# Performance work log

Measured on AMD Instinct MI355X. Metric: run time of the kernel, lower is better.

The kernel has to match this reference:

```python
import math
import jax, jax.numpy as jnp
import numpy as np

B, S, H, BOT, RD, N, K = 4, 2048, 1024, 128, 48, 4096, 8

def setup_inputs() -> dict:
    key = jax.random.key(0)
    ks = jax.random.split(key, 12)
    hidden_states = jax.random.normal(ks[0], (B, S, H), jnp.float32)
    q_proj_w = jax.random.normal(ks[1], (BOT, H), jnp.float32) * (1.0 / math.sqrt(H))
    router_w = jax.random.normal(ks[2], (RD, BOT), jnp.float32) * (1.0 / math.sqrt(BOT))
    aux_keys = jax.random.normal(ks[3], (N, BOT), jnp.float32) * 0.01
    aux_values = jax.random.normal(ks[4], (N, H), jnp.float32) * 0.02
    # reliability per slot (log-domain additive mask derived from lifecycle state)
    reliability_mask = jax.random.uniform(ks[5], (N,), jnp.float32)
    unc_w1 = jax.random.normal(ks[6], (H // 4, H), jnp.float32) * (1.0 / math.sqrt(H))
    unc_b1 = jnp.zeros((H // 4,), jnp.float32)
    unc_w2 = jax.random.normal(ks[7], (1, H // 4), jnp.float32) * 0.02
    unc_b2 = jnp.zeros((1,), jnp.float32)
    gate_w1 = jnp.asarray(0.5, jnp.float32)
    gate_bias = jnp.asarray(-1.0, jnp.float32)
    return {"hidden_states": hidden_states, "q_proj_w": q_proj_w, "router_w": router_w,
            "aux_keys": aux_keys, "aux_values": aux_values, "reliability_mask": reliability_mask,
            "unc_w1": unc_w1, "unc_b1": unc_b1, "unc_w2": unc_w2, "unc_b2": unc_b2,
            "gate_w1": gate_w1, "gate_bias": gate_bias}

def reference(hidden_states, q_proj_w, router_w, aux_keys, aux_values, reliability_mask,
              unc_w1, unc_b1, unc_w2, unc_b2, gate_w1, gate_bias):
    # --- SlotRouter: project query/keys to router_dim, score, mask, top-k ---
    query = jnp.einsum('bsh,dh->bsd', hidden_states, q_proj_w)        # [B,S,BOT]
    rq = jnp.einsum('bsd,rd->bsr', query, router_w)                   # [B,S,RD]
    rk = jnp.einsum('nd,rd->nr', aux_keys, router_w)                  # [N,RD]
    scores = jnp.einsum('bsr,nr->bsn', rq, rk) / math.sqrt(RD)        # [B,S,N]
    scores = scores + reliability_mask[None, None, :]
    top_scores, top_idx = jax.lax.top_k(scores, K)                    # [B,S,K]
    # --- UncertaintyEstimator (HIDDEN_VARIANCE) ---
    mean = hidden_states.mean(axis=-1, keepdims=True)
    variance = ((hidden_states - mean) ** 2).mean(axis=-1)            # [B,S]
    log_var = jnp.log1p(variance)
    normalized_var = log_var / (log_var.mean() + 1e-6)
    h1 = jax.nn.gelu(jnp.einsum('bsh,fh->bsf', hidden_states, unc_w1) + unc_b1, approximate=False)
    learned = (jnp.einsum('bsf,of->bso', h1, unc_w2) + unc_b2)[..., 0]
    uncertainty = jnp.clip(normalized_var * 0.5 + jax.nn.sigmoid(learned) * 2.5, 0.0, 5.0)
    # --- Gate-1 scalar gate + slot aggregation ---
    gate = jax.nn.sigmoid(gate_w1 * uncertainty + gate_bias)          # [B,S]
    w = jax.nn.softmax(top_scores, axis=-1)                           # [B,S,K]
    v = aux_values[top_idx]                                           # [B,S,K,H]
    agg = jnp.einsum('bsk,bskh->bsh', w, v)
    out = hidden_states + gate[..., None] * agg
    return out
```

## Files before the change

kernel.cpp:

```cpp
#include <hip/hip_runtime.h>
#include <hip/hip_bf16.h>
#include <math.h>
#include <stdint.h>

#define NT 256
constexpr int Hc = 1024, BOTc = 128, RDc = 48, Nc = 4096;
constexpr int ROWS = 8192;
constexpr float INV_SQRT_RD = 0.14433756729740643f;

typedef short bf16x8 __attribute__((ext_vector_type(8)));
typedef float f32x4 __attribute__((ext_vector_type(4)));

__device__ __forceinline__ uint32_t umin32(uint32_t a, uint32_t b) { return a < b ? a : b; }
__device__ __forceinline__ uint32_t umax32(uint32_t a, uint32_t b) { return a > b ? a : b; }
__device__ __forceinline__ void ce_asc(uint32_t& x, uint32_t& y) {
  uint32_t lo = umin32(x, y), hi = umax32(x, y); x = lo; y = hi;
}
__device__ __forceinline__ uint32_t pack_score(float s, int slot) {
  uint32_t u = __float_as_uint(s);
  u = (u & 0x80000000u) ? ~u : (u | 0x80000000u);
  return (u & 0xFFFFF000u) | (uint32_t)slot;
}
__device__ __forceinline__ float unpack_score(uint32_t p) {
  uint32_t m = p & 0xFFFFF000u;
  uint32_t f = (m & 0x80000000u) ? (m ^ 0x80000000u) : ~m;
  return __uint_as_float(f);
}
__device__ __forceinline__ void merge_top8(uint32_t a[8], const uint32_t b[8]) {
  uint32_t m[8];
#pragma unroll
  for (int i = 0; i < 8; ++i) m[i] = umax32(a[i], b[7 - i]);
  ce_asc(m[0], m[4]); ce_asc(m[1], m[5]); ce_asc(m[2], m[6]); ce_asc(m[3], m[7]);
  ce_asc(m[0], m[2]); ce_asc(m[1], m[3]); ce_asc(m[4], m[6]); ce_asc(m[5], m[7]);
  ce_asc(m[0], m[1]); ce_asc(m[2], m[3]); ce_asc(m[4], m[5]); ce_asc(m[6], m[7]);
#pragma unroll
  for (int i = 0; i < 8; ++i) a[i] = m[i];
}
__device__ __forceinline__ void top8_insert(uint32_t top[8], uint32_t p) {
  if (p > top[0]) {
    top[0] = p;
    ce_asc(top[0], top[1]); ce_asc(top[1], top[2]); ce_asc(top[2], top[3]);
    ce_asc(top[3], top[4]); ce_asc(top[4], top[5]); ce_asc(top[5], top[6]);
    ce_asc(top[6], top[7]);
  }
}
__device__ __forceinline__ uint16_t bf16bits(float x) {
  uint32_t u = __float_as_uint(x);
  return (uint16_t)(((u + 0x7FFFu + ((u >> 16) & 1u)) >> 16) & 0xFFFFu);
}
__device__ __forceinline__ float bf2f(uint16_t h) {
  return __uint_as_float((uint32_t)h << 16);
}

constexpr int GP_W48 = 64, GP_RK = 768, GP_HB = 1024, GP_CVW = 32, GP_CVA = 512;
__global__ __launch_bounds__(256) void k_prep_all(
    const float* __restrict__ hidden, const float* __restrict__ q_proj_w,
    const float* __restrict__ router_w, const float* __restrict__ aux_keys,
    const float* __restrict__ aux_values, const float* __restrict__ rel,
    const float* __restrict__ unc_w1,
    uint16_t* __restrict__ xb, float* __restrict__ log_var,
    uint16_t* __restrict__ wcat, uint16_t* __restrict__ avb,
    uint16_t* __restrict__ rk_b) {
  int bid = blockIdx.x;
  int tid = threadIdx.x;
  if (bid < GP_W48) {
    __shared__ float rw[BOTc];
    int j = bid;
    if (j >= RDc) {
      for (int hh = tid; hh < Hc; hh += NT) wcat[(size_t)(256 + j) * Hc + hh] = 0;
      return;
    }
    for (int d = tid; d < BOTc; d += NT) rw[d] = router_w[j * BOTc + d];
    __syncthreads();
    float acc[4] = {0.f, 0.f, 0.f, 0.f};
#pragma unroll 4
    for (int d = 0; d < BOTc; ++d) {
      float r = rw[d];
#pragma unroll
      for (int jj = 0; jj < 4; ++jj)
        acc[jj] = fmaf(r, q_proj_w[d * Hc + tid + 256 * jj], acc[jj]);
    }
#pragma unroll
    for (int jj = 0; jj < 4; ++jj)
      wcat[(size_t)(256 + j) * Hc + tid + 256 * jj] = bf16bits(acc[jj]);
    return;
  }
  bid -= GP_W48;
  if (bid < GP_RK) {
    int gid = bid * NT + tid;
    int n = gid / RDc, r = gid - n * RDc;
    float acc = 0.f;
#pragma unroll 8
    for (int d = 0; d < BOTc; ++d)
      acc = fmaf(aux_keys[n * BOTc + d], router_w[r * BOTc + d], acc);
    rk_b[(size_t)n * 64 + r] = bf16bits(acc * INV_SQRT_RD);
    if (r < 16) rk_b[(size_t)n * 64 + 48 + r] = (r == 0) ? bf16bits(rel[n]) : (uint16_t)0;
    return;
  }
  bid -= GP_RK;
  if (bid < GP_HB) {
    int wave = tid >> 6, lane = tid & 63;
    int row = bid * 8 + wave * 2;
    const float4* r0 = reinterpret_cast<const float4*>(hidden + (size_t)row * Hc);
    const float4* r1 = reinterpret_cast<const float4*>(hidden + (size_t)(row + 1) * Hc);
    float4 v0[4], v1[4];
#pragma unroll
    for (int i = 0; i < 4; ++i) v0[i] = r0[lane + 64 * i];
#pragma unroll
    for (int i = 0; i < 4; ++i) v1[i] = r1[lane + 64 * i];
    float s0 = 0.f, q0 = 0.f, s1 = 0.f, q1 = 0.f;
#pragma unroll
    for (int i = 0; i < 4; ++i) {
      ushort4 h;
      h.x = bf16bits(v0[i].x); h.y = bf16bits(v0[i].y);
      h.z = bf16bits(v0[i].z); h.w = bf16bits(v0[i].w);
      *reinterpret_cast<ushort4*>(xb + (size_t)row * Hc + (lane + 64 * i) * 4) = h;
      s0 += v0[i].x + v0[i].y + v0[i].z + v0[i].w;
      q0 += v0[i].x * v0[i].x + v0[i].y * v0[i].y + v0[i].z * v0[i].z + v0[i].w * v0[i].w;
    }
#pragma unroll
    for (int i = 0; i < 4; ++i) {
      ushort4 h;
      h.x = bf16bits(v1[i].x); h.y = bf16bits(v1[i].y);
      h.z = bf16bits(v1[i].z); h.w = bf16bits(v1[i].w);
      *reinterpret_cast<ushort4*>(xb + (size_t)(row + 1) * Hc + (lane + 64 * i) * 4) = h;
      s1 += v1[i].x + v1[i].y + v1[i].z + v1[i].w;
      q1 += v1[i].x * v1[i].x + v1[i].y * v1[i].y + v1[i].z * v1[i].z + v1[i].w * v1[i].w;
    }
#pragma unroll
    for (int d = 32; d >= 1; d >>= 1) {
      s0 += __shfl_down(s0, d); q0 += __shfl_down(q0, d);
      s1 += __shfl_down(s1, d); q1 += __shfl_down(q1, d);
    }
    if (lane == 0) {
      float m0 = s0 * (1.f / Hc), m1 = s1 * (1.f / Hc);
      log_var[row]     = log1pf(q0 * (1.f / Hc) - m0 * m0);
      log_var[row + 1] = log1pf(q1 * (1.f / Hc) - m1 * m1);
    }
    return;
  }
  bid -= GP_HB;
  if (bid < GP_CVW) {
    float4 v[8];
    int base = bid * 2048 + tid;
#pragma unroll
    for (int i = 0; i < 8; ++i) v[i] = reinterpret_cast<const float4*>(unc_w1)[base + i * 256];
#pragma unroll
    for (int i = 0; i < 8; ++i) {
      ushort4 h;
      h.x = bf16bits(v[i].x); h.y = bf16bits(v[i].y);
      h.z = bf16bits(v[i].z); h.w = bf16bits(v[i].w);
      reinterpret_cast<ushort4*>(wcat)[base + i * 256] = h;
    }
    return;
  }
  bid -= GP_CVW;
  {
    float4 v[8];
    int base = bid * 2048 + tid;
#pragma unroll
    for (int i = 0; i < 8; ++i) v[i] = reinterpret_cast<const float4*>(aux_values)[base + i * 256];
#pragma unroll
    for (int i = 0; i < 8; ++i) {
      ushort4 h;
      h.x = bf16bits(v[i].x); h.y = bf16bits(v[i].y);
      h.z = bf16bits(v[i].z); h.w = bf16bits(v[i].w);
      reinterpret_cast<ushort4*>(avb)[base + i * 256] = h;
    }
  }
}

__global__ __launch_bounds__(256) void k_xw(const uint16_t* __restrict__ xb,
                                            const uint16_t* __restrict__ wcat,
                                            const float* __restrict__ b1,
                                            const float* __restrict__ w2,
                                            float* __restrict__ uncp,
                                            uint16_t* __restrict__ rq_b) {
  __shared__ uint16_t As[2][64 * 72];
  __shared__ uint16_t Bs[2][64 * 72];
  int bid = blockIdx.x;
  int wid = (bid & 7) * 80 + (bid >> 3);
  int rowg = wid / 5, colg = wid - rowg * 5;
  int tid = threadIdx.x, wave = tid >> 6, lane = tid & 63;
  int l15 = lane & 15, lg = lane >> 4;
  int wr = wave >> 1, wc = wave & 1;
  int row0 = rowg * 64, n0 = colg * 64;
  int srow = tid >> 3, sseg = tid & 7;
  const uint16_t* agp = xb + (size_t)(row0 + srow) * Hc + sseg * 8;
  const uint16_t* bgp = wcat + (size_t)(n0 + srow) * Hc + sseg * 8;
  int sboff = srow * 72 + sseg * 8;
  int arow = wr * 32 + l15, brow = wc * 32 + l15;

  bf16x8 ra0 = *reinterpret_cast<const bf16x8*>(agp);
  bf16x8 ra1 = *reinterpret_cast<const bf16x8*>(agp + (size_t)32 * Hc);
  bf16x8 rb0 = *reinterpret_cast<const bf16x8*>(bgp);
  bf16x8 rb1 = *reinterpret_cast<const bf16x8*>(bgp + (size_t)32 * Hc);
  f32x4 acc00 = {0.f,0.f,0.f,0.f}, acc01 = {0.f,0.f,0.f,0.f};
  f32x4 acc10 = {0.f,0.f,0.f,0.f}, acc11 = {0.f,0.f,0.f,0.f};

  for (int t = 0; t < 16; ++t) {
    int buf = t & 1;
    *reinterpret_cast<bf16x8*>(&As[buf][sboff]) = ra0;
    *reinterpret_cast<bf16x8*>(&As[buf][sboff + 32 * 72]) = ra1;
    *reinterpret_cast<bf16x8*>(&Bs[buf][sboff]) = rb0;
    *reinterpret_cast<bf16x8*>(&Bs[buf][sboff + 32 * 72]) = rb1;
    if (t < 15) {
      int k0 = (t + 1) * 64;
      ra0 = *reinterpret_cast<const bf16x8*>(agp + k0);
      ra1 = *reinterpret_cast<const bf16x8*>(agp + (size_t)32 * Hc + k0);
      rb0 = *reinterpret_cast<const bf16x8*>(bgp + k0);
      rb1 = *reinterpret_cast<const bf16x8*>(bgp + (size_t)32 * Hc + k0);
    }
    __syncthreads();
#pragma unroll
    for (int ks = 0; ks < 2; ++ks) {
      bf16x8 a0 = *reinterpret_cast<const bf16x8*>(&As[buf][arow * 72 + ks * 32 + lg * 8]);
      bf16x8 a1 = *reinterpret_cast<const bf16x8*>(&As[buf][(arow + 16) * 72 + ks * 32 + lg * 8]);
      bf16x8 b0 = *reinterpret_cast<const bf16x8*>(&Bs[buf][brow * 72 + ks * 32 + lg * 8]);
      bf16x8 b1f = *reinterpret_cast<const bf16x8*>(&Bs[buf][(brow + 16) * 72 + ks * 32 + lg * 8]);
      acc00 = __builtin_amdgcn_mfma_f32_16x16x32_bf16(a0, b0, acc00, 0, 0, 0);
      acc01 = __builtin_amdgcn_mfma_f32_16x16x32_bf16(a0, b1f, acc01, 0, 0, 0);
      acc10 = __builtin_amdgcn_mfma_f32_16x16x32_bf16(a1, b0, acc10, 0, 0, 0);
      acc11 = __builtin_amdgcn_mfma_f32_16x16x32_bf16(a1, b1f, acc11, 0, 0, 0);
    }
    __syncthreads();
  }
  if (colg < 4) {
    int gc0 = n0 + wc * 32 + l15;
    float b1v0 = b1[gc0],      w2v0 = w2[gc0];
    float b1v1 = b1[gc0 + 16], w2v1 = w2[gc0 + 16];
    int strip = colg * 2 + wc;
    float part0[4], part1[4];
#pragma unroll
    for (int r = 0; r < 4; ++r) {
      float x00 = acc00[r] + b1v0, x01 = acc01[r] + b1v1;
      float x10 = acc10[r] + b1v0, x11 = acc11[r] + b1v1;
      float g00 = 0.5f * x00 * (1.f + erff(x00 * 0.70710678118654752f));
      float g01 = 0.5f * x01 * (1.f + erff(x01 * 0.70710678118654752f));
      float g10 = 0.5f * x10 * (1.f + erff(x10 * 0.70710678118654752f));
      float g11 = 0.5f * x11 * (1.f + erff(x11 * 0.70710678118654752f));
      part0[r] = fmaf(g00, w2v0, g01 * w2v1);
      part1[r] = fmaf(g10, w2v0, g11 * w2v1);
    }
#pragma unroll
    for (int d = 1; d < 16; d <<= 1)
#pragma unroll
      for (int r = 0; r < 4; ++r) {
        part0[r] += __shfl_xor(part0[r], d);
        part1[r] += __shfl_xor(part1[r], d);
      }
    if (l15 == 0) {
#pragma unroll
      for (int r = 0; r < 4; ++r) {
        uncp[(size_t)(row0 + wr * 32 + lg * 4 + r) * 8 + strip] = part0[r];
        uncp[(size_t)(row0 + wr * 32 + 16 + lg * 4 + r) * 8 + strip] = part1[r];
      }
    }
  } else {
    int colA = wc * 32 + l15, colB = colA + 16;
#pragma unroll
    for (int r = 0; r < 4; ++r) {
      int rA = row0 + wr * 32 + lg * 4 + r, rB = rA + 16;
      uint16_t vA = bf16bits(acc00[r]);
      uint16_t vB = (colB == 48) ? (uint16_t)0x3F80u : bf16bits(acc01[r]);
      uint16_t uA = bf16bits(acc10[r]);
      uint16_t uB = (colB == 48) ? (uint16_t)0x3F80u : bf16bits(acc11[r]);
      rq_b[(size_t)rA * 64 + colA] = vA;
      rq_b[(size_t)rA * 64 + colB] = vB;
      rq_b[(size_t)rB * 64 + colA] = uA;
      rq_b[(size_t)rB * 64 + colB] = uB;
    }
  }
}

__global__ __launch_bounds__(256) void k_scores_mfma(const uint16_t* __restrict__ rq_b,
                                                     const uint16_t* __restrict__ rk_b,
                                                     uint32_t* __restrict__ cand,
                                                     const float* __restrict__ log_var,
                                                     float* __restrict__ stats) {
  int tid = threadIdx.x;
  if (blockIdx.x == 1024) {
    float s = 0.f;
    for (int i = tid; i < ROWS; i += NT) s += log_var[i];
#pragma unroll
    for (int d = 32; d >= 1; d >>= 1) s += __shfl_down(s, d);
    __shared__ float ls[4];
    int lane = tid & 63, wid = tid >> 6;
    if (lane == 0) ls[wid] = s;
    __syncthreads();
    if (tid == 0) {
      s = ls[0] + ls[1] + ls[2] + ls[3];
      stats[0] = 1.f / (s * (1.f / ROWS) + 1e-6f);
    }
    return;
  }
  int wave = tid >> 6, lane = tid & 63;
  int l15 = lane & 15, lg = lane >> 4;
  int rowg = blockIdx.x >> 3, range = blockIdx.x & 7;
  int q0 = rowg * 64 + wave * 16;
  const uint16_t* qp = rq_b + (size_t)(q0 + l15) * 64 + lg * 8;
  bf16x8 qf1 = *reinterpret_cast<const bf16x8*>(qp);
  bf16x8 qf2 = *reinterpret_cast<const bf16x8*>(qp + 32);
  uint32_t top[8];
#pragma unroll
  for (int q = 0; q < 8; ++q) top[q] = 0u;
  int sbase = range * 512;
  const uint16_t* kp = rk_b + (size_t)(sbase + l15) * 64 + lg * 8;
  bf16x8 a1c = *reinterpret_cast<const bf16x8*>(kp);
  bf16x8 a2c = *reinterpret_cast<const bf16x8*>(kp + 32);
  bf16x8 a3c = *reinterpret_cast<const bf16x8*>(kp + 1024);
  bf16x8 a4c = *reinterpret_cast<const bf16x8*>(kp + 1024 + 32);
#pragma unroll
  for (int t = 0; t < 32; t += 2) {
    bf16x8 a1n, a2n, a3n, a4n;
    if (t < 30) {
      const uint16_t* kpn = kp + (size_t)(t + 2) * 1024;
      a1n = *reinterpret_cast<const bf16x8*>(kpn);
      a2n = *reinterpret_cast<const bf16x8*>(kpn + 32);
      a3n = *reinterpret_cast<const bf16x8*>(kpn + 1024);
      a4n = *reinterpret_cast<const bf16x8*>(kpn + 1024 + 32);
    }
    int s0 = sbase + t * 16;
    f32x4 acc0 = {0.f,0.f,0.f,0.f}, acc1 = {0.f,0.f,0.f,0.f};
    acc0 = __builtin_amdgcn_mfma_f32_16x16x32_bf16(a1c, qf1, acc0, 0, 0, 0);
    acc1 = __builtin_amdgcn_mfma_f32_16x16x32_bf16(a3c, qf1, acc1, 0, 0, 0);
    acc0 = __builtin_amdgcn_mfma_f32_16x16x32_bf16(a2c, qf2, acc0, 0, 0, 0);
    acc1 = __builtin_amdgcn_mfma_f32_16x16x32_bf16(a4c, qf2, acc1, 0, 0, 0);
#pragma unroll
    for (int r = 0; r < 4; ++r) top8_insert(top, pack_score(acc0[r], s0 + lg * 4 + r));
#pragma unroll
    for (int r = 0; r < 4; ++r) top8_insert(top, pack_score(acc1[r], s0 + 16 + lg * 4 + r));
    if (t < 30) { a1c = a1n; a2c = a2n; a3c = a3n; a4c = a4n; }
  }
#pragma unroll
  for (int dd = 16; dd <= 32; dd <<= 1) {
    uint32_t o[8];
#pragma unroll
    for (int q = 0; q < 8; ++q) o[q] = __shfl_xor(top[q], dd);
    merge_top8(top, o);
  }
  if (lg == 0) {
    int row = q0 + l15;
#pragma unroll
    for (int q = 0; q < 8; ++q) cand[((size_t)row * 8 + range) * 8 + q] = top[q];
  }
}

__global__ __launch_bounds__(256) void k_final(const uint16_t* __restrict__ xb,
                                               const uint16_t* __restrict__ avb,
                                               const uint32_t* __restrict__ cand,
                                               const float* __restrict__ log_var,
                                               const float* __restrict__ uncp,
                                               const float* __restrict__ stats,
                                               const float* __restrict__ b2,
                                               const float* __restrict__ gw,
                                               const float* __restrict__ gb,
                                               float* __restrict__ out) {
  int row = blockIdx.x;
  int tid = threadIdx.x;
  __shared__ float ws_[8]; __shared__ int wi_[8]; __shared__ float sgate;
  if (tid < 64) {
    int lane = tid;
    uint32_t l[8];
    float up = 0.f;
    if (lane < 8) {
      const uint32_t* c = cand + (size_t)row * 64 + lane * 8;
#pragma unroll
      for (int q = 0; q < 8; ++q) l[q] = c[q];
      up = uncp[(size_t)row * 8 + lane];
    } else {
#pragma unroll
      for (int q = 0; q < 8; ++q) l[q] = 0u;
    }
#pragma unroll
    for (int d = 1; d < 8; d <<= 1) {
      uint32_t o[8];
#pragma unroll
      for (int q = 0; q < 8; ++q) o[q] = __shfl_xor(l[q], d);
      merge_top8(l, o);
      up += __shfl_xor(up, d);
    }
    if (lane == 0) {
      float sc[8];
#pragma unroll
      for (int q = 0; q < 8; ++q) sc[q] = unpack_score(l[q]);
      float mx = sc[7];
      float e[8]; float sum = 0.f;
#pragma unroll
      for (int q = 0; q < 8; ++q) { e[q] = expf(sc[q] - mx); sum += e[q]; }
      float inv = 1.f / sum;
#pragma unroll
      for (int q = 0; q < 8; ++q) { ws_[q] = e[q] * inv; wi_[q] = (int)(l[q] & 0xFFFu); }
      float learned = up + b2[0];
      float nv = log_var[row] * stats[0];
      float sig = 1.f / (1.f + expf(-learned));
      float u = nv * 0.5f + sig * 2.5f;
      u = fminf(fmaxf(u, 0.f), 5.f);
      sgate = 1.f / (1.f + expf(-(gw[0] * u + gb[0])));
    }
  }
  __syncthreads();
  int h0 = tid * 4;
  ushort4 hb = *reinterpret_cast<const ushort4*>(xb + (size_t)row * Hc + h0);
  float ax = 0.f, ay = 0.f, az = 0.f, aw = 0.f;
#pragma unroll
  for (int k = 0; k < 8; ++k) {
    float w = ws_[k];
    ushort4 v = *reinterpret_cast<const ushort4*>(avb + (size_t)wi_[k] * Hc + h0);
    ax = fmaf(w, bf2f(v.x), ax); ay = fmaf(w, bf2f(v.y), ay);
    az = fmaf(w, bf2f(v.z), az); aw = fmaf(w, bf2f(v.w), aw);
  }
  float g = sgate;
  float4 o;
  o.x = bf2f(hb.x) + g * ax; o.y = bf2f(hb.y) + g * ay;
  o.z = bf2f(hb.z) + g * az; o.w = bf2f(hb.w) + g * aw;
  *reinterpret_cast<float4*>(out + (size_t)row * Hc + h0) = o;
}

extern "C" void kernel_launch(void* const* d_in, const int* in_sizes, int n_in,
                              void* d_out, int out_size, void* d_ws, size_t ws_size,
                              hipStream_t stream) {
  const float* hidden     = (const float*)d_in[0];
  const float* q_proj_w   = (const float*)d_in[1];
  const float* router_w   = (const float*)d_in[2];
  const float* aux_keys   = (const float*)d_in[3];
  const float* aux_values = (const float*)d_in[4];
  const float* rel        = (const float*)d_in[5];
  const float* unc_w1     = (const float*)d_in[6];
  const float* unc_b1     = (const float*)d_in[7];
  const float* unc_w2     = (const float*)d_in[8];
  const float* unc_b2     = (const float*)d_in[9];
  const float* gate_w1    = (const float*)d_in[10];
  const float* gate_bias  = (const float*)d_in[11];
  float* out = (float*)d_out;

  uint8_t* w = (uint8_t*)d_ws;
  uint16_t* xb    = (uint16_t*)w;                 w += (size_t)ROWS * Hc * 2;
  uint16_t* wcat  = (uint16_t*)w;                 w += (size_t)320 * Hc * 2;
  uint16_t* avb   = (uint16_t*)w;                 w += (size_t)Nc * Hc * 2;
  uint16_t* rq_b  = (uint16_t*)w;                 w += (size_t)ROWS * 64 * 2;
  uint16_t* rk_b  = (uint16_t*)w;                 w += (size_t)Nc * 64 * 2;
  float* log_var  = (float*)w;                    w += (size_t)ROWS * 4;
  float* uncp     = (float*)w;                    w += (size_t)ROWS * 8 * 4;
  float* stats    = (float*)w;                    w += 256;
  uint32_t* cand  = (uint32_t*)w;                 w += (size_t)ROWS * 64 * 4;

  k_prep_all<<<GP_W48 + GP_RK + GP_HB + GP_CVW + GP_CVA, NT, 0, stream>>>(
      hidden, q_proj_w, router_w, aux_keys, aux_values, rel, unc_w1,
      xb, log_var, wcat, avb, rk_b);
  k_xw<<<640, NT, 0, stream>>>(xb, wcat, unc_b1, unc_w2, uncp, rq_b);
  k_scores_mfma<<<1025, NT, 0, stream>>>(rq_b, rk_b, cand, log_var, stats);
  k_final<<<ROWS, NT, 0, stream>>>(xb, avb, cand, log_var, uncp,
                                   stats, unc_b2, gate_w1, gate_bias, out);
}
```

Baseline: 98.61 us.

## Deepen GEMM register prefetch, move log_var reduction, batch 4 rows per final block

The k_xw GEMM main loop is unrolled by two with two register staging sets, so global loads run two K-tiles ahead of the shared-memory compute. The log_var mean reduction moves from an extra block in the scores kernel to an extra block in the GEMM kernel. The final aggregation kernel now handles four rows per block, one wave per row for the top-8 merge and gate, cutting block count and launch overhead. The extra prefetch registers may lower occupancy, and each thread now does four rows of sequential gather work.

Result: faster. 92.91 us (median of 2 runs) (-5.8%).

```diff
diff --git a/kernel.cpp b/kernel.cpp
--- a/kernel.cpp
+++ b/kernel.cpp
@@ -174,14 +174,32 @@
                                             const uint16_t* __restrict__ wcat,
                                             const float* __restrict__ b1,
                                             const float* __restrict__ w2,
+                                            const float* __restrict__ log_var,
+                                            float* __restrict__ stats,
                                             float* __restrict__ uncp,
                                             uint16_t* __restrict__ rq_b) {
+  int bid = blockIdx.x;
+  int tid = threadIdx.x;
+  if (bid == 640) {
+    float s = 0.f;
+    for (int i = tid; i < ROWS; i += NT) s += log_var[i];
+#pragma unroll
+    for (int d = 32; d >= 1; d >>= 1) s += __shfl_down(s, d);
+    __shared__ float ls[4];
+    int lane = tid & 63, wv = tid >> 6;
+    if (lane == 0) ls[wv] = s;
+    __syncthreads();
+    if (tid == 0) {
+      s = ls[0] + ls[1] + ls[2] + ls[3];
+      stats[0] = 1.f / (s * (1.f / ROWS) + 1e-6f);
+    }
+    return;
+  }
   __shared__ uint16_t As[2][64 * 72];
   __shared__ uint16_t Bs[2][64 * 72];
-  int bid = blockIdx.x;
   int wid = (bid & 7) * 80 + (bid >> 3);
   int rowg = wid / 5, colg = wid - rowg * 5;
-  int tid = threadIdx.x, wave = tid >> 6, lane = tid & 63;
+  int wave = tid >> 6, lane = tid & 63;
   int l15 = lane & 15, lg = lane >> 4;
   int wr = wave >> 1, wc = wave & 1;
   int row0 = rowg * 64, n0 = colg * 64;
@@ -191,39 +209,64 @@
   int sboff = srow * 72 + sseg * 8;
   int arow = wr * 32 + l15, brow = wc * 32 + l15;
 
-  bf16x8 ra0 = *reinterpret_cast<const bf16x8*>(agp);
-  bf16x8 ra1 = *reinterpret_cast<const bf16x8*>(agp + (size_t)32 * Hc);
-  bf16x8 rb0 = *reinterpret_cast<const bf16x8*>(bgp);
-  bf16x8 rb1 = *reinterpret_cast<const bf16x8*>(bgp + (size_t)32 * Hc);
+  bf16x8 a0A = *reinterpret_cast<const bf16x8*>(agp);
+  bf16x8 a1A = *reinterpret_cast<const bf16x8*>(agp + (size_t)32 * Hc);
+  bf16x8 b0A = *reinterpret_cast<const bf16x8*>(bgp);
+  bf16x8 b1A = *reinterpret_cast<const bf16x8*>(bgp + (size_t)32 * Hc);
+  bf16x8 a0B = *reinterpret_cast<const bf16x8*>(agp + 64);
+  bf16x8 a1B = *reinterpret_cast<const bf16x8*>(agp + (size_t)32 * Hc + 64);
+  bf16x8 b0B = *reinterpret_cast<const bf16x8*>(bgp + 64);
+  bf16x8 b1B = *reinterpret_cast<const bf16x8*>(bgp + (size_t)32 * Hc + 64);
   f32x4 acc00 = {0.f,0.f,0.f,0.f}, acc01 = {0.f,0.f,0.f,0.f};
   f32x4 acc10 = {0.f,0.f,0.f,0.f}, acc11 = {0.f,0.f,0.f,0.f};
 
-  for (int t = 0; t < 16; ++t) {
-    int buf = t & 1;
-    *reinterpret_cast<bf16x8*>(&As[buf][sboff]) = ra0;
-    *reinterpret_cast<bf16x8*>(&As[buf][sboff + 32 * 72]) = ra1;
-    *reinterpret_cast<bf16x8*>(&Bs[buf][sboff]) = rb0;
-    *reinterpret_cast<bf16x8*>(&Bs[buf][sboff + 32 * 72]) = rb1;
-    if (t < 15) {
-      int k0 = (t + 1) * 64;
-      ra0 = *reinterpret_cast<const bf16x8*>(agp + k0);
-      ra1 = *reinterpret_cast<const bf16x8*>(agp + (size_t)32 * Hc + k0);
-      rb0 = *reinterpret_cast<const bf16x8*>(bgp + k0);
-      rb1 = *reinterpret_cast<const bf16x8*>(bgp + (size_t)32 * Hc + k0);
+  for (int tt = 0; tt < 16; tt += 2) {
+    *reinterpret_cast<bf16x8*>(&As[0][sboff]) = a0A;
+    *reinterpret_cast<bf16x8*>(&As[0][sboff + 32 * 72]) = a1A;
+    *reinterpret_cast<bf16x8*>(&Bs[0][sboff]) = b0A;
+    *reinterpret_cast<bf16x8*>(&Bs[0][sboff + 32 * 72]) = b1A;
+    if (tt + 2 < 16) {
+      int k0 = (tt + 2) * 64;
+      a0A = *reinterpret_cast<const bf16x8*>(agp + k0);
+      a1A = *reinterpret_cast<const bf16x8*>(agp + (size_t)32 * Hc + k0);
+      b0A = *reinterpret_cast<const bf16x8*>(bgp + k0);
+      b1A = *reinterpret_cast<const bf16x8*>(bgp + (size_t)32 * Hc + k0);
     }
     __syncthreads();
 #pragma unroll
     for (int ks = 0; ks < 2; ++ks) {
-      bf16x8 a0 = *reinterpret_cast<const bf16x8*>(&As[buf][arow * 72 + ks * 32 + lg * 8]);
-      bf16x8 a1 = *reinterpret_cast<const bf16x8*>(&As[buf][(arow + 16) * 72 + ks * 32 + lg * 8]);
-      bf16x8 b0 = *reinterpret_cast<const bf16x8*>(&Bs[buf][brow * 72 + ks * 32 + lg * 8]);
-      bf16x8 b1f = *reinterpret_cast<const bf16x8*>(&Bs[buf][(brow + 16) * 72 + ks * 32 + lg * 8]);
+      bf16x8 a0 = *reinterpret_cast<const bf16x8*>(&As[0][arow * 72 + ks * 32 + lg * 8]);
+      bf16x8 a1 = *reinterpret_cast<const bf16x8*>(&As[0][(arow + 16) * 72 + ks * 32 + lg * 8]);
+      bf16x8 b0 = *reinterpret_cast<const bf16x8*>(&Bs[0][brow * 72 + ks * 32 + lg * 8]);
+      bf16x8 b1f = *reinterpret_cast<const bf16x8*>(&Bs[0][(brow + 16) * 72 + ks * 32 + lg * 8]);
       acc00 = __builtin_amdgcn_mfma_f32_16x16x32_bf16(a0, b0, acc00, 0, 0, 0);
       acc01 = __builtin_amdgcn_mfma_f32_16x16x32_bf16(a0, b1f, acc01, 0, 0, 0);
       acc10 = __builtin_amdgcn_mfma_f32_16x16x32_bf16(a1, b0, acc10, 0, 0, 0);
       acc11 = __builtin_amdgcn_mfma_f32_16x16x32_bf16(a1, b1f, acc11, 0, 0, 0);
     }
+    *reinterpret_cast<bf16x8*>(&As[1][sboff]) = a0B;
+    *reinterpret_cast<bf16x8*>(&As[1][sboff + 32 * 72]) = a1B;
+    *reinterpret_cast<bf16x8*>(&Bs[1][sboff]) = b0B;
+    *reinterpret_cast<bf16x8*>(&Bs[1][sboff + 32 * 72]) = b1B;
+    if (tt + 3 < 16) {
+      int k0 = (tt + 3) * 64;
+      a0B = *reinterpret_cast<const bf16x8*>(agp + k0);
+      a1B = *reinterpret_cast<const bf16x8*>(agp + (size_t)32 * Hc + k0);
+      b0B = *reinterpret_cast<const bf16x8*>(bgp + k0);
+      b1B = *reinterpret_cast<const bf16x8*>(bgp + (size_t)32 * Hc + k0);
+    }
     __syncthreads();
+#pragma unroll
+    for (int ks = 0; ks < 2; ++ks) {
+      bf16x8 a0 = *reinterpret_cast<const bf16x8*>(&As[1][arow * 72 + ks * 32 + lg * 8]);
+      bf16x8 a1 = *reinterpret_cast<const bf16x8*>(&As[1][(arow + 16) * 72 + ks * 32 + lg * 8]);
+      bf16x8 b0 = *reinterpret_cast<const bf16x8*>(&Bs[1][brow * 72 + ks * 32 + lg * 8]);
+      bf16x8 b1f = *reinterpret_cast<const bf16x8*>(&Bs[1][(brow + 16) * 72 + ks * 32 + lg * 8]);
+      acc00 = __builtin_amdgcn_mfma_f32_16x16x32_bf16(a0, b0, acc00, 0, 0, 0);
+      acc01 = __builtin_amdgcn_mfma_f32_16x16x32_bf16(a0, b1f, acc01, 0, 0, 0);
+      acc10 = __builtin_amdgcn_mfma_f32_16x16x32_bf16(a1, b0, acc10, 0, 0, 0);
+      acc11 = __builtin_amdgcn_mfma_f32_16x16x32_bf16(a1, b1f, acc11, 0, 0, 0);
+    }
   }
   if (colg < 4) {
     int gc0 = n0 + wc * 32 + l15;
@@ -275,25 +318,8 @@
 
 __global__ __launch_bounds__(256) void k_scores_mfma(const uint16_t* __restrict__ rq_b,
                                                      const uint16_t* __restrict__ rk_b,
-                                                     uint32_t* __restrict__ cand,
-                                                     const float* __restrict__ log_var,
-                                                     float* __restrict__ stats) {
+                                                     uint32_t* __restrict__ cand) {
   int tid = threadIdx.x;
-  if (blockIdx.x == 1024) {
-    float s = 0.f;
-    for (int i = tid; i < ROWS; i += NT) s += log_var[i];
-#pragma unroll
-    for (int d = 32; d >= 1; d >>= 1) s += __shfl_down(s, d);
-    __shared__ float ls[4];
-    int lane = tid & 63, wid = tid >> 6;
-    if (lane == 0) ls[wid] = s;
-    __syncthreads();
-    if (tid == 0) {
-      s = ls[0] + ls[1] + ls[2] + ls[3];
-      stats[0] = 1.f / (s * (1.f / ROWS) + 1e-6f);
-    }
-    return;
-  }
   int wave = tid >> 6, lane = tid & 63;
   int l15 = lane & 15, lg = lane >> 4;
   int rowg = blockIdx.x >> 3, range = blockIdx.x & 7;
@@ -356,11 +382,12 @@
                                                const float* __restrict__ gw,
                                                const float* __restrict__ gb,
                                                float* __restrict__ out) {
-  int row = blockIdx.x;
   int tid = threadIdx.x;
-  __shared__ float ws_[8]; __shared__ int wi_[8]; __shared__ float sgate;
-  if (tid < 64) {
-    int lane = tid;
+  int wave = tid >> 6, lane = tid & 63;
+  int row0 = blockIdx.x * 4;
+  __shared__ float ws_[4][8]; __shared__ int wi_[4][8]; __shared__ float sg[4];
+  {
+    int row = row0 + wave;
     uint32_t l[8];
     float up = 0.f;
     if (lane < 8) {
@@ -390,31 +417,35 @@
       for (int q = 0; q < 8; ++q) { e[q] = expf(sc[q] - mx); sum += e[q]; }
       float inv = 1.f / sum;
 #pragma unroll
-      for (int q = 0; q < 8; ++q) { ws_[q] = e[q] * inv; wi_[q] = (int)(l[q] & 0xFFFu); }
+      for (int q = 0; q < 8; ++q) { ws_[wave][q] = e[q] * inv; wi_[wave][q] = (int)(l[q] & 0xFFFu); }
       float learned = up + b2[0];
       float nv = log_var[row] * stats[0];
       float sig = 1.f / (1.f + expf(-learned));
       float u = nv * 0.5f + sig * 2.5f;
       u = fminf(fmaxf(u, 0.f), 5.f);
-      sgate = 1.f / (1.f + expf(-(gw[0] * u + gb[0])));
+      sg[wave] = 1.f / (1.f + expf(-(gw[0] * u + gb[0])));
     }
   }
   __syncthreads();
   int h0 = tid * 4;
-  ushort4 hb = *reinterpret_cast<const ushort4*>(xb + (size_t)row * Hc + h0);
-  float ax = 0.f, ay = 0.f, az = 0.f, aw = 0.f;
-#pragma unroll
-  for (int k = 0; k < 8; ++k) {
-    float w = ws_[k];
-    ushort4 v = *reinterpret_cast<const ushort4*>(avb + (size_t)wi_[k] * Hc + h0);
-    ax = fmaf(w, bf2f(v.x), ax); ay = fmaf(w, bf2f(v.y), ay);
-    az = fmaf(w, bf2f(v.z), az); aw = fmaf(w, bf2f(v.w), aw);
-  }
-  float g = sgate;
-  float4 o;
-  o.x = bf2f(hb.x) + g * ax; o.y = bf2f(hb.y) + g * ay;
-  o.z = bf2f(hb.z) + g * az; o.w = bf2f(hb.w) + g * aw;
-  *reinterpret_cast<float4*>(out + (size_t)row * Hc + h0) = o;
+#pragma unroll
+  for (int rr = 0; rr < 4; ++rr) {
+    int row = row0 + rr;
+    ushort4 hb = *reinterpret_cast<const ushort4*>(xb + (size_t)row * Hc + h0);
+    float ax = 0.f, ay = 0.f, az = 0.f, aw = 0.f;
+#pragma unroll
+    for (int k = 0; k < 8; ++k) {
+      float w = ws_[rr][k];
+      ushort4 v = *reinterpret_cast<const ushort4*>(avb + (size_t)wi_[rr][k] * Hc + h0);
+      ax = fmaf(w, bf2f(v.x), ax); ay = fmaf(w, bf2f(v.y), ay);
+      az = fmaf(w, bf2f(v.z), az); aw = fmaf(w, bf2f(v.w), aw);
+    }
+    float g = sg[rr];
+    float4 o;
+    o.x = bf2f(hb.x) + g * ax; o.y = bf2f(hb.y) + g * ay;
+    o.z = bf2f(hb.z) + g * az; o.w = bf2f(hb.w) + g * aw;
+    *reinterpret_cast<float4*>(out + (size_t)row * Hc + h0) = o;
+  }
 }
 
 extern "C" void kernel_launch(void* const* d_in, const int* in_sizes, int n_in,
@@ -448,8 +479,8 @@
   k_prep_all<<<GP_W48 + GP_RK + GP_HB + GP_CVW + GP_CVA, NT, 0, stream>>>(
       hidden, q_proj_w, router_w, aux_keys, aux_values, rel, unc_w1,
       xb, log_var, wcat, avb, rk_b);
-  k_xw<<<640, NT, 0, stream>>>(xb, wcat, unc_b1, unc_w2, uncp, rq_b);
-  k_scores_mfma<<<1025, NT, 0, stream>>>(rq_b, rk_b, cand, log_var, stats);
-  k_final<<<ROWS, NT, 0, stream>>>(xb, avb, cand, log_var, uncp,
-                                   stats, unc_b2, gate_w1, gate_bias, out);
-}
+  k_xw<<<641, NT, 0, stream>>>(xb, wcat, unc_b1, unc_w2, log_var, stats, uncp, rq_b);
+  k_scores_mfma<<<1024, NT, 0, stream>>>(rq_b, rk_b, cand);
+  k_final<<<ROWS / 4, NT, 0, stream>>>(xb, avb, cand, log_var, uncp,
+                                       stats, unc_b2, gate_w1, gate_bias, out);
+}
```
